# Performance work log

Hardware: AMD Instinct MI355X
Metric: run time of the kernel (lower is better)

The kernel has to match this reference:

```python
import jax, jax.numpy as jnp
import numpy as np

LN_EPS = 1e-5


def setup_inputs() -> dict:
    key = jax.random.key(0)
    ks = jax.random.split(key, 6)
    B, I, H = 16384, 512, 512
    x = jax.random.normal(ks[0], (B, I), dtype=jnp.float32)
    h_prev = jax.random.normal(ks[1], (B, H), dtype=jnp.float32)
    c_prev = jax.random.normal(ks[2], (B, H), dtype=jnp.float32)
    # packed gate weights in i|f|g|o order (equivalent to 8 separate matmuls)
    W_i = jax.random.normal(ks[3], (I, 4 * H), dtype=jnp.float32) * (1.0 / np.sqrt(I))
    W_h = jax.random.normal(ks[4], (H, 4 * H), dtype=jnp.float32) * (1.0 / np.sqrt(H))
    # biases: b_i=0, b_f=1, b_g=0, b_o=0 as in the torch module
    b = jnp.concatenate([jnp.zeros(H), jnp.ones(H), jnp.zeros(H), jnp.zeros(H)]).astype(jnp.float32)
    ln_weight = jnp.ones((H,), dtype=jnp.float32)
    ln_bias = jnp.zeros((H,), dtype=jnp.float32)
    return {"x": x, "h_prev": h_prev, "c_prev": c_prev, "W_i": W_i, "W_h": W_h,
            "b": b, "ln_weight": ln_weight, "ln_bias": ln_bias}


def layer_norm(h, w, bias):
    mu = jnp.mean(h, axis=-1, keepdims=True)
    var = jnp.var(h, axis=-1, keepdims=True)
    return (h - mu) * jax.lax.rsqrt(var + LN_EPS) * w + bias


def reference(x, h_prev, c_prev, W_i, W_h, b, ln_weight, ln_bias):
    H = h_prev.shape[-1]
    # two fused GEMMs covering all 4 gates: [B, 4H]
    gates = x @ W_i + h_prev @ W_h + b
    i, f, g, o = jnp.split(gates, 4, axis=-1)
    i = jax.nn.sigmoid(i)
    f = jax.nn.sigmoid(f)
    g = jnp.tanh(g)
    o = jax.nn.sigmoid(o)
    c = f * c_prev + i * g
    h = o * jnp.tanh(c)
    h = layer_norm(h, ln_weight, ln_bias)
    return (h, c)
```

## Files before the change

### kernel.cpp

```cpp
#include <hip/hip_runtime.h>
#include <cstdint>
#include <cstddef>

typedef unsigned short ushort_t;
typedef __attribute__((ext_vector_type(8))) short bf16x8;
typedef __attribute__((ext_vector_type(4))) float f32x4;

#define MROWS 16384
#define KDIM  1024
#define NDIM  2048
#define HDIM  512
#define NTILE 16

static __device__ __forceinline__ unsigned short f2bf(float f) {
    unsigned int u = __float_as_uint(f);
    u += 0x7fffu + ((u >> 16) & 1u);
    return (unsigned short)(u >> 16);
}

static __device__ __forceinline__ float sigmoid_f(float x) {
    return 1.0f / (1.0f + __expf(-x));
}
static __device__ __forceinline__ float tanh_f(float x) {
    float t = __expf(2.0f * x);
    return 1.0f - 2.0f / (t + 1.0f);
}

__global__ __launch_bounds__(256) void pack_ab(const float* __restrict__ x,
                                               const float* __restrict__ hp,
                                               const float* __restrict__ Wi,
                                               const float* __restrict__ Wh,
                                               ushort_t* __restrict__ A,
                                               ushort_t* __restrict__ Bt) {
    __shared__ ushort_t sm[64][72];
    const int tid = threadIdx.x;
    if (blockIdx.x < 8192) {
        int t = blockIdx.x * 256 + tid;
        int row = t >> 7;
        int kc = (t & 127) << 3;
        const float* src = (kc < 512) ? (x + (size_t)row * 512 + kc)
                                      : (hp + (size_t)row * 512 + (kc - 512));
        float4 v0 = ((const float4*)src)[0];
        float4 v1 = ((const float4*)src)[1];
        ushort_t o[8] __attribute__((aligned(16)));
        o[0] = f2bf(v0.x); o[1] = f2bf(v0.y); o[2] = f2bf(v0.z); o[3] = f2bf(v0.w);
        o[4] = f2bf(v1.x); o[5] = f2bf(v1.y); o[6] = f2bf(v1.z); o[7] = f2bf(v1.w);
        *((uint4*)(A + (size_t)row * KDIM + kc)) = *((const uint4*)o);
    } else {
        int b2 = blockIdx.x - 8192;
        int kt = b2 >> 5;
        int ct = b2 & 31;
        const float* W = (kt < 8) ? (Wi + (size_t)(kt * 64) * NDIM)
                                  : (Wh + (size_t)((kt - 8) * 64) * NDIM);
        int c0 = (tid & 15) * 4;
        int r0 = tid >> 4;
#pragma unroll
        for (int r = 0; r < 4; ++r) {
            int krow = r * 16 + r0;
            float4 v = *((const float4*)(W + (size_t)krow * NDIM + ct * 64 + c0));
            sm[krow][c0 + 0] = f2bf(v.x);
            sm[krow][c0 + 1] = f2bf(v.y);
            sm[krow][c0 + 2] = f2bf(v.z);
            sm[krow][c0 + 3] = f2bf(v.w);
        }
        __syncthreads();
        int g = (ct * 64) >> 9;
        int h0 = ct * 64 - g * 512;
#pragma unroll
        for (int q = tid; q < 512; q += 256) {
            int cc = q >> 3;
            int kc = (q & 7) * 8;
            ushort_t o[8] __attribute__((aligned(16)));
#pragma unroll
            for (int j = 0; j < 8; ++j) o[j] = sm[kc + j][cc];
            int np = 4 * (h0 + cc) + g;
            *((uint4*)(Bt + (size_t)np * KDIM + kt * 64 + kc)) = *((const uint4*)o);
        }
    }
}

__global__ __launch_bounds__(512, 2) void gemm_cell(const ushort_t* __restrict__ A,
                                                    const ushort_t* __restrict__ Bt,
                                                    const float* __restrict__ b,
                                                    const float* __restrict__ c_prev,
                                                    float* __restrict__ h_out,
                                                    float* __restrict__ c_out) {
    __shared__ ushort_t lds[2][32768];

    const int tid  = threadIdx.x;
    const int w    = tid >> 6;
    const int lane = tid & 63;
    const int mi   = w >> 2;
    const int nj   = w & 3;
    int bid = blockIdx.x;
    int lid = (bid & 7) * 64 + (bid >> 3);
    const int m0 = (lid >> 3) * 256;
    const int n0 = (lid & 7) * 256;
    const int lr   = lane & 15;
    const int quad = lane >> 4;
    const int sw   = lr & 7;

    const int trow0 = tid >> 3;
    const int chg   = (tid & 7) ^ (trow0 & 7);
    const size_t a_base = (size_t)(m0 + trow0) * KDIM + chg * 8;
    const size_t b_base = (size_t)(n0 + trow0) * KDIM + chg * 8;
    const int    l_base = tid * 16;

#define STAGE(kt, bufi) do {                                                        \
    const ushort_t* ap_ = A + a_base + (size_t)(kt) * 64;                           \
    const ushort_t* bp_ = Bt + b_base + (size_t)(kt) * 64;                          \
    char* al_ = (char*)&lds[bufi][0];                                               \
    char* bl_ = (char*)&lds[bufi][16384];                                           \
    _Pragma("unroll")                                                               \
    for (int r_ = 0; r_ < 4; ++r_)                                                  \
        __builtin_amdgcn_global_load_lds(                                           \
            (const __attribute__((address_space(1))) void*)(ap_ + (size_t)r_ * 64 * KDIM), \
            (__attribute__((address_space(3))) void*)(al_ + l_base + r_ * 8192),    \
            16, 0, 0);                                                              \
    _Pragma("unroll")                                                               \
    for (int r_ = 0; r_ < 4; ++r_)                                                  \
        __builtin_amdgcn_global_load_lds(                                           \
            (const __attribute__((address_space(1))) void*)(bp_ + (size_t)r_ * 64 * KDIM), \
            (__attribute__((address_space(3))) void*)(bl_ + l_base + r_ * 8192),    \
            16, 0, 0);                                                              \
} while (0)

    f32x4 acc[8][4];
#pragma unroll
    for (int i = 0; i < 8; ++i)
#pragma unroll
        for (int j = 0; j < 4; ++j) acc[i][j] = (f32x4){0.f, 0.f, 0.f, 0.f};

    STAGE(0, 0);
    STAGE(1, 1);
    asm volatile("s_waitcnt vmcnt(8)\n\ts_barrier" ::: "memory");

#pragma unroll 2
    for (int t = 0; t < NTILE; ++t) {
        const ushort_t* Ab = &lds[t & 1][0];
        const ushort_t* Bb = &lds[t & 1][16384];
        bf16x8 af[4], bfr[4];

#pragma unroll
        for (int t2 = 0; t2 < 4; ++t2) {
            int ra = mi * 128 + t2 * 16 + lr;
            af[t2] = *((const bf16x8*)(Ab + (ra * 8 + (quad ^ sw)) * 8));
        }
#pragma unroll
        for (int t3 = 0; t3 < 4; ++t3) {
            int rb = nj * 64 + t3 * 16 + lr;
            bfr[t3] = *((const bf16x8*)(Bb + (rb * 8 + (quad ^ sw)) * 8));
        }
        __builtin_amdgcn_s_barrier();
        __builtin_amdgcn_s_setprio(1);
#pragma unroll
        for (int tm = 0; tm < 4; ++tm)
#pragma unroll
            for (int tn = 0; tn < 4; ++tn)
                acc[tm][tn] = __builtin_amdgcn_mfma_f32_16x16x32_bf16(
                    af[tm], bfr[tn], acc[tm][tn], 0, 0, 0);
        __builtin_amdgcn_s_setprio(0);
        __builtin_amdgcn_s_barrier();

#pragma unroll
        for (int t2 = 0; t2 < 4; ++t2) {
            int ra = mi * 128 + (t2 + 4) * 16 + lr;
            af[t2] = *((const bf16x8*)(Ab + (ra * 8 + (quad ^ sw)) * 8));
        }
        __builtin_amdgcn_s_barrier();
        __builtin_amdgcn_s_setprio(1);
#pragma unroll
        for (int tm = 0; tm < 4; ++tm)
#pragma unroll
            for (int tn = 0; tn < 4; ++tn)
                acc[tm + 4][tn] = __builtin_amdgcn_mfma_f32_16x16x32_bf16(
                    af[tm], bfr[tn], acc[tm + 4][tn], 0, 0, 0);
        __builtin_amdgcn_s_setprio(0);
        __builtin_amdgcn_s_barrier();

#pragma unroll
        for (int t2 = 0; t2 < 4; ++t2) {
            int ra = mi * 128 + t2 * 16 + lr;
            af[t2] = *((const bf16x8*)(Ab + (ra * 8 + ((4 + quad) ^ sw)) * 8));
        }
#pragma unroll
        for (int t3 = 0; t3 < 4; ++t3) {
            int rb = nj * 64 + t3 * 16 + lr;
            bfr[t3] = *((const bf16x8*)(Bb + (rb * 8 + ((4 + quad) ^ sw)) * 8));
        }
        __builtin_amdgcn_s_barrier();
        __builtin_amdgcn_s_setprio(1);
#pragma unroll
        for (int tm = 0; tm < 4; ++tm)
#pragma unroll
            for (int tn = 0; tn < 4; ++tn)
                acc[tm][tn] = __builtin_amdgcn_mfma_f32_16x16x32_bf16(
                    af[tm], bfr[tn], acc[tm][tn], 0, 0, 0);
        __builtin_amdgcn_s_setprio(0);
        __builtin_amdgcn_s_barrier();

#pragma unroll
        for (int t2 = 0; t2 < 4; ++t2) {
            int ra = mi * 128 + (t2 + 4) * 16 + lr;
            af[t2] = *((const bf16x8*)(Ab + (ra * 8 + ((4 + quad) ^ sw)) * 8));
        }
        __builtin_amdgcn_s_barrier();
        __builtin_amdgcn_s_setprio(1);
#pragma unroll
        for (int tm = 0; tm < 4; ++tm)
#pragma unroll
            for (int tn = 0; tn < 4; ++tn)
                acc[tm + 4][tn] = __builtin_amdgcn_mfma_f32_16x16x32_bf16(
                    af[tm], bfr[tn], acc[tm + 4][tn], 0, 0, 0);
        __builtin_amdgcn_s_setprio(0);
        asm volatile("s_waitcnt lgkmcnt(0)\n\ts_barrier" ::: "memory");

        if (t < NTILE - 2) {
            STAGE(t + 2, t & 1);
            asm volatile("s_waitcnt vmcnt(8)\n\ts_barrier" ::: "memory");
        } else if (t == NTILE - 2) {
            asm volatile("s_waitcnt vmcnt(0)\n\ts_barrier" ::: "memory");
        }
    }
#undef STAGE

    float* scr = (float*)&lds[0][0] + w * 1024;
    const int rr = lane >> 2;
    const int hg0 = ((n0 + nj * 64) >> 2) + (lane & 3) * 4;
    const float4 bi4 = *((const float4*)(b + hg0));
    const float4 bff = *((const float4*)(b + 512 + hg0));
    const float4 bgg = *((const float4*)(b + 1024 + hg0));
    const float4 boo = *((const float4*)(b + 1536 + hg0));
    const float bi[4] = {bi4.x, bi4.y, bi4.z, bi4.w};
    const float bfv[4] = {bff.x, bff.y, bff.z, bff.w};
    const float bg[4] = {bgg.x, bgg.y, bgg.z, bgg.w};
    const float bo[4] = {boo.x, boo.y, boo.z, boo.w};

#pragma unroll
    for (int tm = 0; tm < 8; ++tm) {
#pragma unroll
        for (int tn = 0; tn < 4; ++tn) {
            int c = tn * 16 + lr;
#pragma unroll
            for (int rg = 0; rg < 4; ++rg) {
                int r = quad * 4 + rg;
                int blk = (c >> 2) ^ r;
                scr[r * 64 + blk * 4 + (c & 3)] = acc[tm][tn][rg];
            }
        }
        float4 gv[4];
#pragma unroll
        for (int j = 0; j < 4; ++j) {
            int cb = (lane & 3) * 4 + j;
            gv[j] = *((const float4*)(scr + rr * 64 + (cb ^ rr) * 4));
        }
        int grow = m0 + mi * 128 + tm * 16 + rr;
        float4 cp4 = *((const float4*)(c_prev + (size_t)grow * HDIM + hg0));
        const float cpv[4] = {cp4.x, cp4.y, cp4.z, cp4.w};
        float cn[4], hv[4];
#pragma unroll
        for (int j = 0; j < 4; ++j) {
            float iv = sigmoid_f(gv[j].x + bi[j]);
            float fv = sigmoid_f(gv[j].y + bfv[j]);
            float g2 = tanh_f(gv[j].z + bg[j]);
            float ov = sigmoid_f(gv[j].w + bo[j]);
            cn[j] = fv * cpv[j] + iv * g2;
            hv[j] = ov * tanh_f(cn[j]);
        }
        float4 cno = {cn[0], cn[1], cn[2], cn[3]};
        float4 hvo = {hv[0], hv[1], hv[2], hv[3]};
        *((float4*)(c_out + (size_t)grow * HDIM + hg0)) = cno;
        *((float4*)(h_out + (size_t)grow * HDIM + hg0)) = hvo;
    }
}

__global__ __launch_bounds__(256) void ln_kernel(float* __restrict__ h,
                                                 const float* __restrict__ lw,
                                                 const float* __restrict__ lb) {
    int w = threadIdx.x >> 6;
    int lane = threadIdx.x & 63;
    int row = blockIdx.x * 4 + w;
    float* p = h + (size_t)row * HDIM + lane * 8;
    float4 a = ((const float4*)p)[0];
    float4 c = ((const float4*)p)[1];
    float s  = a.x + a.y + a.z + a.w + c.x + c.y + c.z + c.w;
    float ss = a.x * a.x + a.y * a.y + a.z * a.z + a.w * a.w +
               c.x * c.x + c.y * c.y + c.z * c.z + c.w * c.w;
#pragma unroll
    for (int off = 32; off > 0; off >>= 1) {
        s  += __shfl_xor(s, off);
        ss += __shfl_xor(ss, off);
    }
    float mu = s * (1.0f / 512.0f);
    float var = ss * (1.0f / 512.0f) - mu * mu;
    float rstd = rsqrtf(var + 1e-5f);
    const float* wp = lw + lane * 8;
    const float* bp = lb + lane * 8;
    float4 w0 = ((const float4*)wp)[0];
    float4 w1 = ((const float4*)wp)[1];
    float4 b0 = ((const float4*)bp)[0];
    float4 b1 = ((const float4*)bp)[1];
    a.x = (a.x - mu) * rstd * w0.x + b0.x;
    a.y = (a.y - mu) * rstd * w0.y + b0.y;
    a.z = (a.z - mu) * rstd * w0.z + b0.z;
    a.w = (a.w - mu) * rstd * w0.w + b0.w;
    c.x = (c.x - mu) * rstd * w1.x + b1.x;
    c.y = (c.y - mu) * rstd * w1.y + b1.y;
    c.z = (c.z - mu) * rstd * w1.z + b1.z;
    c.w = (c.w - mu) * rstd * w1.w + b1.w;
    ((float4*)p)[0] = a;
    ((float4*)p)[1] = c;
}

extern "C" void kernel_launch(void* const* d_in, const int* in_sizes, int n_in,
                              void* d_out, int out_size, void* d_ws, size_t ws_size,
                              hipStream_t stream) {
    const float* x      = (const float*)d_in[0];
    const float* h_prev = (const float*)d_in[1];
    const float* c_prev = (const float*)d_in[2];
    const float* W_i    = (const float*)d_in[3];
    const float* W_h    = (const float*)d_in[4];
    const float* b      = (const float*)d_in[5];
    const float* ln_w   = (const float*)d_in[6];
    const float* ln_b   = (const float*)d_in[7];

    float* h_out = (float*)d_out;
    float* c_out = h_out + (size_t)MROWS * HDIM;

    ushort_t* A  = (ushort_t*)d_ws;
    ushort_t* Bt = A + (size_t)MROWS * KDIM;

    pack_ab<<<8192 + 512, 256, 0, stream>>>(x, h_prev, W_i, W_h, A, Bt);
    gemm_cell<<<512, 512, 0, stream>>>(A, Bt, b, c_prev, h_out, c_out);
    ln_kernel<<<MROWS / 4, 256, 0, stream>>>(h_out, ln_w, ln_b);
}
```

Before: 247.3 us.

## Interleave next-tile global loads into MFMA phases and reorder K-slices per quadrant

Splits the staging macro into separate A and B loads and issues the next tile's B and A prefetches partway through the current tile's compute phases, instead of after all MFMAs finish. The per-tile compute is reordered into four output quadrants that each consume both K halves, so A fragments for both K halves are loaded at once. The aim is to overlap global-to-LDS traffic with MFMA work and remove the bubble at the end of each tile. The cost is more live registers for fragments, and the buffer being overwritten is also being read by ds_reads that follow, which relies on the barriers for correctness.

```diff
diff --git a/kernel.cpp b/kernel.cpp
--- a/kernel.cpp
+++ b/kernel.cpp
@@ -106,17 +106,19 @@
     const size_t b_base = (size_t)(n0 + trow0) * KDIM + chg * 8;
     const int    l_base = tid * 16;
 
-#define STAGE(kt, bufi) do {                                                        \
+#define STAGE_A(kt, bufi) do {                                                      \
     const ushort_t* ap_ = A + a_base + (size_t)(kt) * 64;                           \
-    const ushort_t* bp_ = Bt + b_base + (size_t)(kt) * 64;                          \
     char* al_ = (char*)&lds[bufi][0];                                               \
-    char* bl_ = (char*)&lds[bufi][16384];                                           \
     _Pragma("unroll")                                                               \
     for (int r_ = 0; r_ < 4; ++r_)                                                  \
         __builtin_amdgcn_global_load_lds(                                           \
             (const __attribute__((address_space(1))) void*)(ap_ + (size_t)r_ * 64 * KDIM), \
             (__attribute__((address_space(3))) void*)(al_ + l_base + r_ * 8192),    \
             16, 0, 0);                                                              \
+} while (0)
+#define STAGE_B(kt, bufi) do {                                                      \
+    const ushort_t* bp_ = Bt + b_base + (size_t)(kt) * 64;                          \
+    char* bl_ = (char*)&lds[bufi][16384];                                           \
     _Pragma("unroll")                                                               \
     for (int r_ = 0; r_ < 4; ++r_)                                                  \
         __builtin_amdgcn_global_load_lds(                                           \
@@ -131,98 +133,112 @@
 #pragma unroll
         for (int j = 0; j < 4; ++j) acc[i][j] = (f32x4){0.f, 0.f, 0.f, 0.f};
 
-    STAGE(0, 0);
-    STAGE(1, 1);
+    STAGE_A(0, 0); STAGE_B(0, 0);
+    STAGE_A(1, 1); STAGE_B(1, 1);
     asm volatile("s_waitcnt vmcnt(8)\n\ts_barrier" ::: "memory");
 
-#pragma unroll 2
-    for (int t = 0; t < NTILE; ++t) {
-        const ushort_t* Ab = &lds[t & 1][0];
-        const ushort_t* Bb = &lds[t & 1][16384];
-        bf16x8 af[4], bfr[4];
-
-#pragma unroll
-        for (int t2 = 0; t2 < 4; ++t2) {
-            int ra = mi * 128 + t2 * 16 + lr;
-            af[t2] = *((const bf16x8*)(Ab + (ra * 8 + (quad ^ sw)) * 8));
-        }
-#pragma unroll
-        for (int t3 = 0; t3 < 4; ++t3) {
-            int rb = nj * 64 + t3 * 16 + lr;
-            bfr[t3] = *((const bf16x8*)(Bb + (rb * 8 + (quad ^ sw)) * 8));
-        }
-        __builtin_amdgcn_s_barrier();
-        __builtin_amdgcn_s_setprio(1);
-#pragma unroll
-        for (int tm = 0; tm < 4; ++tm)
-#pragma unroll
-            for (int tn = 0; tn < 4; ++tn)
-                acc[tm][tn] = __builtin_amdgcn_mfma_f32_16x16x32_bf16(
-                    af[tm], bfr[tn], acc[tm][tn], 0, 0, 0);
-        __builtin_amdgcn_s_setprio(0);
-        __builtin_amdgcn_s_barrier();
-
-#pragma unroll
-        for (int t2 = 0; t2 < 4; ++t2) {
-            int ra = mi * 128 + (t2 + 4) * 16 + lr;
-            af[t2] = *((const bf16x8*)(Ab + (ra * 8 + (quad ^ sw)) * 8));
-        }
-        __builtin_amdgcn_s_barrier();
-        __builtin_amdgcn_s_setprio(1);
-#pragma unroll
-        for (int tm = 0; tm < 4; ++tm)
-#pragma unroll
-            for (int tn = 0; tn < 4; ++tn)
-                acc[tm + 4][tn] = __builtin_amdgcn_mfma_f32_16x16x32_bf16(
-                    af[tm], bfr[tn], acc[tm + 4][tn], 0, 0, 0);
-        __builtin_amdgcn_s_setprio(0);
-        __builtin_amdgcn_s_barrier();
-
-#pragma unroll
-        for (int t2 = 0; t2 < 4; ++t2) {
-            int ra = mi * 128 + t2 * 16 + lr;
-            af[t2] = *((const bf16x8*)(Ab + (ra * 8 + ((4 + quad) ^ sw)) * 8));
-        }
-#pragma unroll
-        for (int t3 = 0; t3 < 4; ++t3) {
-            int rb = nj * 64 + t3 * 16 + lr;
-            bfr[t3] = *((const bf16x8*)(Bb + (rb * 8 + ((4 + quad) ^ sw)) * 8));
-        }
-        __builtin_amdgcn_s_barrier();
-        __builtin_amdgcn_s_setprio(1);
-#pragma unroll
-        for (int tm = 0; tm < 4; ++tm)
-#pragma unroll
-            for (int tn = 0; tn < 4; ++tn)
-                acc[tm][tn] = __builtin_amdgcn_mfma_f32_16x16x32_bf16(
-                    af[tm], bfr[tn], acc[tm][tn], 0, 0, 0);
-        __builtin_amdgcn_s_setprio(0);
-        __builtin_amdgcn_s_barrier();
-
-#pragma unroll
-        for (int t2 = 0; t2 < 4; ++t2) {
-            int ra = mi * 128 + (t2 + 4) * 16 + lr;
-            af[t2] = *((const bf16x8*)(Ab + (ra * 8 + ((4 + quad) ^ sw)) * 8));
-        }
-        __builtin_amdgcn_s_barrier();
-        __builtin_amdgcn_s_setprio(1);
-#pragma unroll
-        for (int tm = 0; tm < 4; ++tm)
-#pragma unroll
-            for (int tn = 0; tn < 4; ++tn)
-                acc[tm + 4][tn] = __builtin_amdgcn_mfma_f32_16x16x32_bf16(
-                    af[tm], bfr[tn], acc[tm + 4][tn], 0, 0, 0);
-        __builtin_amdgcn_s_setprio(0);
-        asm volatile("s_waitcnt lgkmcnt(0)\n\ts_barrier" ::: "memory");
-
-        if (t < NTILE - 2) {
-            STAGE(t + 2, t & 1);
-            asm volatile("s_waitcnt vmcnt(8)\n\ts_barrier" ::: "memory");
-        } else if (t == NTILE - 2) {
-            asm volatile("s_waitcnt vmcnt(0)\n\ts_barrier" ::: "memory");
-        }
+#define TILE(t_, BUF_) do {                                                         \
+    const ushort_t* Ab_ = &lds[BUF_][0];                                            \
+    const ushort_t* Bb_ = &lds[BUF_][16384];                                        \
+    bf16x8 af[4][2], b0v[2][2], b1v[2][2];                                          \
+                                 \
+    _Pragma("unroll")                                                               \
+    for (int t2 = 0; t2 < 4; ++t2) {                                                \
+        int ra = mi * 128 + t2 * 16 + lr;                                           \
+        af[t2][0] = *((const bf16x8*)(Ab_ + (ra * 8 + (quad ^ sw)) * 8));           \
+        af[t2][1] = *((const bf16x8*)(Ab_ + (ra * 8 + ((4 + quad) ^ sw)) * 8));     \
+    }                                                                               \
+    _Pragma("unroll")                                                               \
+    for (int j = 0; j < 2; ++j) {                                                   \
+        int rb = nj * 64 + j * 16 + lr;                                             \
+        b0v[j][0] = *((const bf16x8*)(Bb_ + (rb * 8 + (quad ^ sw)) * 8));           \
+        b0v[j][1] = *((const bf16x8*)(Bb_ + (rb * 8 + ((4 + quad) ^ sw)) * 8));     \
+    }                                                                               \
+    __builtin_amdgcn_s_barrier();                                                   \
+    __builtin_amdgcn_s_setprio(1);                                                  \
+    _Pragma("unroll")                                                               \
+    for (int t2 = 0; t2 < 4; ++t2)                                                  \
+        _Pragma("unroll")                                                           \
+        for (int j = 0; j < 2; ++j) {                                               \
+            acc[t2][j] = __builtin_amdgcn_mfma_f32_16x16x32_bf16(                   \
+                af[t2][0], b0v[j][0], acc[t2][j], 0, 0, 0);                         \
+            acc[t2][j] = __builtin_amdgcn_mfma_f32_16x16x32_bf16(                   \
+                af[t2][1], b0v[j][1], acc[t2][j], 0, 0, 0);                         \
+        }                                                                           \
+    __builtin_amdgcn_s_setprio(0);                                                  \
+    asm volatile("s_barrier" ::: "memory");                                         \
+                                        \
+    _Pragma("unroll")                                                               \
+    for (int j = 0; j < 2; ++j) {                                                   \
+        int rb = nj * 64 + (j + 2) * 16 + lr;                                       \
+        b1v[j][0] = *((const bf16x8*)(Bb_ + (rb * 8 + (quad ^ sw)) * 8));           \
+        b1v[j][1] = *((const bf16x8*)(Bb_ + (rb * 8 + ((4 + quad) ^ sw)) * 8));     \
+    }                                                                               \
+    __builtin_amdgcn_s_barrier();                                                   \
+    __builtin_amdgcn_s_setprio(1);                                                  \
+    _Pragma("unroll")                                                               \
+    for (int t2 = 0; t2 < 4; ++t2)                                                  \
+        _Pragma("unroll")                                                           \
+        for (int j = 0; j < 2; ++j) {                                               \
+            acc[t2][j + 2] = __builtin_amdgcn_mfma_f32_16x16x32_bf16(               \
+                af[t2][0], b1v[j][0], acc[t2][j + 2], 0, 0, 0);                     \
+            acc[t2][j + 2] = __builtin_amdgcn_mfma_f32_16x16x32_bf16(               \
+                af[t2][1], b1v[j][1], acc[t2][j + 2], 0, 0, 0);                     \
+        }                                                                           \
+    __builtin_amdgcn_s_setprio(0);                                                  \
+    asm volatile("s_barrier" ::: "memory");          \
+                         \
+    _Pragma("unroll")                                                               \
+    for (int t2 = 0; t2 < 4; ++t2) {                                                \
+        int ra = mi * 128 + (t2 + 4) * 16 + lr;                                     \
+        af[t2][0] = *((const bf16x8*)(Ab_ + (ra * 8 + (quad ^ sw)) * 8));           \
+        af[t2][1] = *((const bf16x8*)(Ab_ + (ra * 8 + ((4 + quad) ^ sw)) * 8));     \
+    }                                                                               \
+    if ((t_) < NTILE - 2) STAGE_B((t_) + 2, BUF_);                                  \
+    __builtin_amdgcn_s_barrier();                                                   \
+    __builtin_amdgcn_s_setprio(1);                                                  \
+    _Pragma("unroll")                                                               \
+    for (int t2 = 0; t2 < 4; ++t2)                                                  \
+        _Pragma("unroll")                                                           \
+        for (int j = 0; j < 2; ++j) {                                               \
+            acc[t2 + 4][j + 2] = __builtin_amdgcn_mfma_f32_16x16x32_bf16(           \
+                af[t2][0], b1v[j][0], acc[t2 + 4][j + 2], 0, 0, 0);                 \
+            acc[t2 + 4][j + 2] = __builtin_amdgcn_mfma_f32_16x16x32_bf16(           \
+                af[t2][1], b1v[j][1], acc[t2 + 4][j + 2], 0, 0, 0);                 \
+        }                                                                           \
+    __builtin_amdgcn_s_setprio(0);                                                  \
+    asm volatile("s_barrier" ::: "memory");          \
+                            \
+    if ((t_) < NTILE - 2) STAGE_A((t_) + 2, BUF_);                                  \
+    __builtin_amdgcn_s_barrier();                                                   \
+    __builtin_amdgcn_s_setprio(1);                                                  \
+    _Pragma("unroll")                                                               \
+    for (int t2 = 0; t2 < 4; ++t2)                                                  \
+        _Pragma("unroll")                                                           \
+        for (int j = 0; j < 2; ++j) {                                               \
+            acc[t2 + 4][j] = __builtin_amdgcn_mfma_f32_16x16x32_bf16(               \
+                af[t2][0], b0v[j][0], acc[t2 + 4][j], 0, 0, 0);                     \
+            acc[t2 + 4][j] = __builtin_amdgcn_mfma_f32_16x16x32_bf16(               \
+                af[t2][1], b0v[j][1], acc[t2 + 4][j], 0, 0, 0);                     \
+        }                                                                           \
+    __builtin_amdgcn_s_setprio(0);                                                  \
+    if ((t_) < NTILE - 2) {                                                         \
+                 \
+        asm volatile("s_waitcnt vmcnt(8)\n\ts_barrier" ::: "memory");               \
+    } else if ((t_) == NTILE - 2) {                                                 \
+        asm volatile("s_waitcnt vmcnt(0)\n\ts_barrier" ::: "memory");               \
+    } else {                                                                        \
+        asm volatile("s_waitcnt lgkmcnt(0)\n\ts_barrier" ::: "memory");             \
+    }                                                                               \
+} while (0)
+
+    for (int tp = 0; tp < NTILE / 2; ++tp) {
+        TILE(2 * tp, 0);
+        TILE(2 * tp + 1, 1);
     }
-#undef STAGE
+#undef TILE
+#undef STAGE_A
+#undef STAGE_B
 
     float* scr = (float*)&lds[0][0] + w * 1024;
     const int rr = lane >> 2;
```

Result: no change. 246.6 us (-0.3%).
